# Kernel optimization log

Measured on AMD Instinct MI355X. Metric: run time of the kernel, lower is better.

The kernel has to match this reference:

```python
import jax, jax.numpy as jnp
import numpy as np

H = W = 32
C = 384
NH = 12
HEAD = C // NH
SCALE = HEAD ** -0.5
WS = 8            # window size
SS = 4            # shift size
N = WS * WS       # tokens per window (64)
NW = (H // WS) * (W // WS)  # windows per image (16)
HIDDEN = 4 * C
EPS = 1e-5
SQRT_2_OVER_PI = float(np.sqrt(2.0 / np.pi))


def _relative_position_index():
    ch = np.arange(WS)
    coords = np.stack(np.meshgrid(ch, ch, indexing='ij')).reshape(2, -1)  # [2, N]
    rel = (coords[:, :, None] - coords[:, None, :]).transpose(1, 2, 0)    # [N, N, 2]
    rel[:, :, 0] += WS - 1
    rel[:, :, 1] += WS - 1
    rel[:, :, 0] *= 2 * WS - 1
    return rel.sum(-1)  # [N, N] int


def _attn_mask():
    img = np.zeros((H, W), np.float32)
    sl = (slice(0, -WS), slice(-WS, -SS), slice(-SS, None))
    cnt = 0
    for hs in sl:
        for ws_ in sl:
            img[hs, ws_] = cnt
            cnt += 1
    m = img.reshape(H // WS, WS, W // WS, WS).transpose(0, 2, 1, 3).reshape(-1, N)  # [nW, N]
    am = m[:, None, :] - m[:, :, None]
    return np.where(am != 0, -100.0, 0.0).astype(np.float32)  # [nW, N, N]


REL_IDX = jnp.asarray(_relative_position_index())
ATTN_MASK = jnp.asarray(_attn_mask())


def _gelu(x):
    return x * 0.5 * (1.0 + jnp.tanh(SQRT_2_OVER_PI * (x + 0.044715 * x ** 3)))


def _layernorm(x, g, b):
    mu = jnp.mean(x, axis=-1, keepdims=True)
    var = jnp.mean(jnp.square(x - mu), axis=-1, keepdims=True)
    return (x - mu) * jax.lax.rsqrt(var + EPS) * g + b


def _window_partition(x):  # [B,H,W,C] -> [B*nW, N, C]
    B = x.shape[0]
    x = x.reshape(B, H // WS, WS, W // WS, WS, C).transpose(0, 1, 3, 2, 4, 5)
    return x.reshape(-1, N, C)


def _window_reverse(w, B):  # [B*nW, N, C] -> [B,H,W,C]
    x = w.reshape(B, H // WS, W // WS, WS, WS, C).transpose(0, 1, 3, 2, 4, 5)
    return x.reshape(B, H, W, C)


def setup_inputs() -> dict:
    key = jax.random.key(0)
    ks = jax.random.split(key, 16)
    s = 0.02
    return {
        'x': jax.random.normal(ks[0], (32, H * W, C), jnp.float32),
        'norm1_g': jnp.ones((C,), jnp.float32),
        'norm1_b': jnp.zeros((C,), jnp.float32),
        'qkv_w': jax.random.normal(ks[1], (C, 3 * C), jnp.float32) * s,
        'qkv_b': jnp.zeros((3 * C,), jnp.float32),
        'rel_bias_table': jax.random.normal(ks[2], ((2 * WS - 1) ** 2, NH), jnp.float32) * s,
        'proj_w': jax.random.normal(ks[3], (C, C), jnp.float32) * s,
        'proj_b': jnp.zeros((C,), jnp.float32),
        'norm2_g': jnp.ones((C,), jnp.float32),
        'norm2_b': jnp.zeros((C,), jnp.float32),
        'fc1_w': jax.random.normal(ks[4], (C, HIDDEN), jnp.float32) * s,
        'fc1_b': jnp.zeros((HIDDEN,), jnp.float32),
        'fc2_w': jax.random.normal(ks[5], (HIDDEN, C), jnp.float32) * s,
        'fc2_b': jnp.zeros((C,), jnp.float32),
    }


def reference(x, norm1_g, norm1_b, qkv_w, qkv_b, rel_bias_table, proj_w, proj_b,
              norm2_g, norm2_b, fc1_w, fc1_b, fc2_w, fc2_b):
    B = x.shape[0]
    shortcut = x
    y = _layernorm(x, norm1_g, norm1_b).reshape(B, H, W, C)
    y = jnp.roll(y, shift=(-SS, -SS), axis=(1, 2))          # cyclic shift
    win = _window_partition(y)                               # [B*nW, N, C]

    qkv = (win @ qkv_w + qkv_b).reshape(-1, N, 3, NH, HEAD).transpose(2, 0, 3, 1, 4)
    q, k, v = qkv[0], qkv[1], qkv[2]                         # [B*nW, NH, N, HEAD]
    attn = jnp.einsum('whnd,whmd->whnm', q * SCALE, k)       # [B*nW, NH, N, N]

    bias = rel_bias_table[REL_IDX.reshape(-1)].reshape(N, N, NH).transpose(2, 0, 1)
    attn = attn + bias[None]
    attn = attn.reshape(B, NW, NH, N, N) + ATTN_MASK[None, :, None]
    attn = jax.nn.softmax(attn.reshape(-1, NH, N, N), axis=-1)

    out = jnp.einsum('whnm,whmd->wnhd', attn, v).reshape(-1, N, C)
    out = out @ proj_w + proj_b                              # [B*nW, N, C]

    y = _window_reverse(out, B)
    y = jnp.roll(y, shift=(SS, SS), axis=(1, 2)).reshape(B, H * W, C)

    x = shortcut + y                                         # drop_path is identity (eval)
    h = _layernorm(x, norm2_g, norm2_b)
    h = _gelu(h @ fc1_w + fc1_b) @ fc2_w + fc2_b
    return x + h
```

## Files before the change

kernel.cpp:

```cpp
#include <hip/hip_runtime.h>
#include <hip/hip_bf16.h>
#include <math.h>

typedef __hip_bfloat16 bf16;
typedef __attribute__((ext_vector_type(8))) short short8;
typedef __attribute__((ext_vector_type(4))) float floatx4;

static constexpr int TOK = 32768;
static constexpr int CDIM = 384;
static constexpr int HID = 1536;

__device__ __forceinline__ bf16 f2bf(float v) { return __float2bfloat16(v); }

__device__ __forceinline__ unsigned short bf_bits(float a) {
  bf16 h = __float2bfloat16(a);
  unsigned short u;
  __builtin_memcpy(&u, &h, 2);
  return u;
}
__device__ __forceinline__ unsigned pack2(float a, float b) {
  return (unsigned)bf_bits(a) | ((unsigned)bf_bits(b) << 16);
}

typedef const __attribute__((address_space(1))) unsigned gas_t;
typedef __attribute__((address_space(3))) unsigned las_t;
__device__ __forceinline__ void gload16(const bf16* g, const bf16* l) {
  __builtin_amdgcn_global_load_lds((gas_t*)g, (las_t*)l, 16, 0, 0);
}

__global__ __launch_bounds__(256) void k_convt4(
    const float* __restrict__ s0, bf16* __restrict__ d0,
    const float* __restrict__ s1, bf16* __restrict__ d1,
    const float* __restrict__ s2, bf16* __restrict__ d2,
    const float* __restrict__ s3, bf16* __restrict__ d3) {
  int tid = blockIdx.x * 256 + threadIdx.x;
  const float* src; bf16* dst; int Kd, Nd, off;
  if (tid < 442368) { src = s0; dst = d0; Kd = 384; Nd = 1152; off = tid; }
  else if (tid < 589824) { src = s1; dst = d1; Kd = 384; Nd = 384; off = tid - 442368; }
  else if (tid < 1179648) { src = s2; dst = d2; Kd = 384; Nd = 1536; off = tid - 589824; }
  else { src = s3; dst = d3; Kd = 1536; Nd = 384; off = tid - 1179648; }
  int k = off / Nd, n = off - k * Nd;
  dst[(size_t)n * Kd + k] = f2bf(src[off]);
}

__global__ __launch_bounds__(256) void k_ln1(const float* __restrict__ x,
                                             const float* __restrict__ g,
                                             const float* __restrict__ b,
                                             bf16* __restrict__ out) {
  int wt = blockIdx.x * 4 + (threadIdx.x >> 6);
  int lane = threadIdx.x & 63;
  int win = wt >> 6, ntok = wt & 63;
  int bimg = win >> 4, wi = win & 15;
  int sh = (((wi >> 2) << 3) + (ntok >> 3) + 4) & 31;
  int sw = (((wi & 3) << 3) + (ntok & 7) + 4) & 31;
  const float* xr = x + ((size_t)bimg * 1024 + sh * 32 + sw) * CDIM;
  float v[6]; float s = 0.f, ss = 0.f;
#pragma unroll
  for (int j = 0; j < 6; ++j) {
    float t = xr[j * 64 + lane];
    v[j] = t; s += t; ss += t * t;
  }
#pragma unroll
  for (int off = 32; off > 0; off >>= 1) {
    s += __shfl_xor(s, off, 64);
    ss += __shfl_xor(ss, off, 64);
  }
  float mu = s * (1.f / 384.f);
  float var = ss * (1.f / 384.f) - mu * mu;
  float rs = rsqrtf(var + 1e-5f);
  bf16* orow = out + (size_t)wt * CDIM;
#pragma unroll
  for (int j = 0; j < 6; ++j) {
    int c = j * 64 + lane;
    orow[c] = f2bf((v[j] - mu) * rs * g[c] + b[c]);
  }
}

__global__ __launch_bounds__(256) void k_ln2(const float* __restrict__ x1,
                                             const float* __restrict__ g,
                                             const float* __restrict__ b,
                                             bf16* __restrict__ out) {
  int t = blockIdx.x * 4 + (threadIdx.x >> 6);
  int lane = threadIdx.x & 63;
  const float* xr = x1 + (size_t)t * CDIM;
  float v[6]; float s = 0.f, ss = 0.f;
#pragma unroll
  for (int j = 0; j < 6; ++j) {
    float q = xr[j * 64 + lane];
    v[j] = q; s += q; ss += q * q;
  }
#pragma unroll
  for (int off = 32; off > 0; off >>= 1) {
    s += __shfl_xor(s, off, 64);
    ss += __shfl_xor(ss, off, 64);
  }
  float mu = s * (1.f / 384.f);
  float var = ss * (1.f / 384.f) - mu * mu;
  float rs = rsqrtf(var + 1e-5f);
  bf16* orow = out + (size_t)t * CDIM;
#pragma unroll
  for (int j = 0; j < 6; ++j) {
    int c = j * 64 + lane;
    orow[c] = f2bf((v[j] - mu) * rs * g[c] + b[c]);
  }
}

template <int K, int EPI, int NT>
__global__ __launch_bounds__(256) void k_gemm(const bf16* __restrict__ A,
                                              const bf16* __restrict__ Bt,
                                              const float* __restrict__ bias,
                                              const float* __restrict__ extra,
                                              void* __restrict__ outp) {
  __shared__ __attribute__((aligned(16))) char pool[49152];
  bf16* A0 = (bf16*)pool;
  bf16* B0 = (bf16*)(pool + 8192);
  bf16* A1 = (bf16*)(pool + 16384);
  bf16* B1 = (bf16*)(pool + 24576);
  bf16* A2 = (bf16*)(pool + 32768);
  bf16* B2 = (bf16*)(pool + 40960);

  const int tid = threadIdx.x;
  const int wv = tid >> 6, lane = tid & 63;

  const int flat = blockIdx.x;
  const int xcd = flat & 7;
  const int idx = flat >> 3;
  const int rpx = (gridDim.x >> 3) / NT;
  const int cb = idx % NT;
  const int rb = idx / NT;
  const int mblk = (xcd * rpx + rb) * 128, nblk = cb * 128;

  const int srow = lane >> 3;
  const int sc = (lane & 7) ^ srow;
  const int srow2 = 2 * srow + (sc >> 2);
  const int gco = (sc & 3) * 8;
  const bf16* gaw = A + (size_t)(mblk + wv * 32 + srow2) * K + gco;
  const bf16* gbw = Bt + (size_t)(nblk + wv * 32 + srow2) * K + gco;
  bf16* lA0 = A0 + wv * 1024; bf16* lB0 = B0 + wv * 1024;
  bf16* lA1 = A1 + wv * 1024; bf16* lB1 = B1 + wv * 1024;
  bf16* lA2 = A2 + wv * 1024; bf16* lB2 = B2 + wv * 1024;

  const int wr = wv >> 1, wc = wv & 1;
  const int mr = lane & 15, q = lane >> 4;
  const int slot8 = ((((mr & 1) << 2) | q) ^ (mr >> 1)) * 8;
  const int faOff = (wr * 32 + (mr >> 1)) * 64 + slot8;
  const int fbOff = (wc * 32 + (mr >> 1)) * 64 + slot8;

  floatx4 acc[4][4];
#pragma unroll
  for (int i = 0; i < 4; ++i)
#pragma unroll
    for (int j = 0; j < 4; ++j) acc[i][j] = floatx4{0.f, 0.f, 0.f, 0.f};

#define VM4() asm volatile("s_waitcnt vmcnt(4)" ::: "memory")
#define VM0() asm volatile("s_waitcnt vmcnt(0)" ::: "memory")
#define BAR() __builtin_amdgcn_s_barrier()

#define STAGE(LA, LB, KOFF) do { \
    gload16(gaw + (KOFF), (LA)); \
    gload16(gaw + (KOFF) + 16 * K, (LA) + 512); \
    gload16(gbw + (KOFF), (LB)); \
    gload16(gbw + (KOFF) + 16 * K, (LB) + 512); \
  } while (0)

#define COMPUTE(ABASE, BBASE) do { \
    short8 a_[4], b_[4]; \
    _Pragma("unroll") \
    for (int mt = 0; mt < 4; ++mt) a_[mt] = *(const short8*)((ABASE) + faOff + mt * 512); \
    _Pragma("unroll") \
    for (int nt = 0; nt < 4; ++nt) b_[nt] = *(const short8*)((BBASE) + fbOff + nt * 512); \
    _Pragma("unroll") \
    for (int mt = 0; mt < 4; ++mt) \
      _Pragma("unroll") \
      for (int nt = 0; nt < 4; ++nt) \
        acc[mt][nt] = __builtin_amdgcn_mfma_f32_16x16x32_bf16(a_[mt], b_[nt], acc[mt][nt], 0, 0, 0); \
  } while (0)

  STAGE(lA0, lB0, 0);
  STAGE(lA1, lB1, 32);
  for (int k0 = 0; k0 < K - 96; k0 += 96) {
    VM4(); BAR(); STAGE(lA2, lB2, k0 + 64);  COMPUTE(A0, B0);
    VM4(); BAR(); STAGE(lA0, lB0, k0 + 96);  COMPUTE(A1, B1);
    VM4(); BAR(); STAGE(lA1, lB1, k0 + 128); COMPUTE(A2, B2);
  }
  VM4(); BAR(); STAGE(lA2, lB2, K - 32); COMPUTE(A0, B0);
  VM4(); BAR();                          COMPUTE(A1, B1);
  VM0(); BAR();                          COMPUTE(A2, B2);
#undef STAGE
#undef COMPUTE
#undef VM4
#undef VM0
#undef BAR

  __syncthreads();
  float* epsw = (float*)pool + wv * (16 * 68);
  const int rr = lane >> 2, c0 = (lane & 3) * 16;
#pragma unroll
  for (int mt = 0; mt < 4; ++mt) {
#pragma unroll
    for (int nt = 0; nt < 4; ++nt)
#pragma unroll
      for (int r = 0; r < 4; ++r)
        epsw[(q * 4 + r) * 68 + nt * 16 + mr] = acc[mt][nt][r];
    float v[16];
#pragma unroll
    for (int j = 0; j < 4; ++j) {
      float4 t = *(const float4*)&epsw[rr * 68 + c0 + j * 4];
      v[j * 4 + 0] = t.x; v[j * 4 + 1] = t.y; v[j * 4 + 2] = t.z; v[j * 4 + 3] = t.w;
    }
    const int grow = mblk + wr * 64 + mt * 16 + rr;
    const int gcol = nblk + wc * 64 + c0;

    if constexpr (EPI == 0) {
      int win = grow >> 6, ntok = grow & 63;
      int s = gcol / 384;
      int rem = gcol - s * 384;
      int h = rem >> 5, d0 = rem & 31;
      bf16* op = (bf16*)outp + (((size_t)s * 512 + win) * 12 + h) * 2048 + ntok * 32 + d0;
      uint4 pk;
      float bv[16];
#pragma unroll
      for (int j = 0; j < 16; ++j) bv[j] = v[j] + bias[gcol + j];
      pk.x = pack2(bv[0], bv[1]); pk.y = pack2(bv[2], bv[3]);
      pk.z = pack2(bv[4], bv[5]); pk.w = pack2(bv[6], bv[7]);
      *(uint4*)op = pk;
      pk.x = pack2(bv[8], bv[9]); pk.y = pack2(bv[10], bv[11]);
      pk.z = pack2(bv[12], bv[13]); pk.w = pack2(bv[14], bv[15]);
      *(uint4*)(op + 8) = pk;
    } else if constexpr (EPI == 1) {
      int win = grow >> 6, ntok = grow & 63;
      int bimg = win >> 4, wi = win & 15;
      int hh = (((wi >> 2) << 3) + (ntok >> 3) + 4) & 31;
      int ww = (((wi & 3) << 3) + (ntok & 7) + 4) & 31;
      size_t t = (size_t)bimg * 1024 + hh * 32 + ww;
      float* op = (float*)outp + t * CDIM + gcol;
      const float* xr = extra + t * CDIM + gcol;
#pragma unroll
      for (int j = 0; j < 4; ++j) {
        float4 xv = *(const float4*)(xr + j * 4);
        float4 ov;
        ov.x = xv.x + v[j * 4 + 0] + bias[gcol + j * 4 + 0];
        ov.y = xv.y + v[j * 4 + 1] + bias[gcol + j * 4 + 1];
        ov.z = xv.z + v[j * 4 + 2] + bias[gcol + j * 4 + 2];
        ov.w = xv.w + v[j * 4 + 3] + bias[gcol + j * 4 + 3];
        *(float4*)(op + j * 4) = ov;
      }
    }
  }
}

__global__ __launch_bounds__(512, 2) void k_mlp(const bf16* __restrict__ A,
                                                const bf16* __restrict__ W1t,
                                                const bf16* __restrict__ W2t,
                                                const float* __restrict__ b1,
                                                const float* __restrict__ b2,
                                                const float* __restrict__ x1,
                                                float* __restrict__ out) {
  __shared__ __attribute__((aligned(16))) char pool[131072];
  bf16* A0 = (bf16*)pool;
  bf16* A1 = (bf16*)(pool + 8192);
  bf16* A2 = (bf16*)(pool + 16384);
  bf16* W10 = (bf16*)(pool + 24576);
  bf16* W11 = (bf16*)(pool + 32768);
  bf16* W12 = (bf16*)(pool + 40960);
  bf16* hs = (bf16*)(pool + 49152);
  bf16* W2sA = (bf16*)(pool + 81920);
  bf16* W2sB = (bf16*)(pool + 106496);

  const int tid = threadIdx.x;
  const int wv = tid >> 6, lane = tid & 63;
  const int mblk = blockIdx.x * 128;

  const int srow = lane >> 3;
  const int sc = (lane & 7) ^ srow;
  const int srow2 = 2 * srow + (sc >> 2);
  const int gco = (sc & 3) * 8;

  const bf16* ga = A + (size_t)(mblk + wv * 16 + srow2) * 384 + gco;
  const bf16* g1 = W1t + (size_t)(wv * 16 + srow2) * 384 + gco;
  const bf16* g2 = W2t + (size_t)(wv * 48 + srow2) * 1536 + gco;

  const int wr1 = wv >> 2, wc1 = wv & 3;
  const int mr = lane & 15, q = lane >> 4;
  const int slot8 = ((((mr & 1) << 2) | q) ^ (mr >> 1)) * 8;
  const int faOff1 = (wr1 * 32 + (mr >> 1)) * 64 + slot8;
  const int fbOff1 = (wc1 * 16 + (mr >> 1)) * 64 + slot8;
  const int fbOff2 = (wc1 * 48 + (mr >> 1)) * 64 + slot8;
  const size_t hb = (size_t)(wr1 * 64 + mr) * 128;
  int px[4];
#pragma unroll
  for (int kk = 0; kk < 4; ++kk)
    px[kk] = (((kk & 2) << 2) | ((((kk & 1) << 2) | q) ^ (mr & 7))) * 8;

  floatx4 acc1[4][2];
  floatx4 acc2[4][6];
#pragma unroll
  for (int i = 0; i < 4; ++i) {
#pragma unroll
    for (int j = 0; j < 2; ++j) acc1[i][j] = floatx4{0.f, 0.f, 0.f, 0.f};
#pragma unroll
    for (int j = 0; j < 6; ++j) acc2[i][j] = floatx4{0.f, 0.f, 0.f, 0.f};
  }

#define VMW(N) asm volatile("s_waitcnt vmcnt(" #N ")" ::: "memory")
#define LGKM0() asm volatile("s_waitcnt lgkmcnt(0)" ::: "memory")
#define BARR() __builtin_amdgcn_s_barrier()
#define ST(ABUF, WBUF, G1P, KO) do { \
    gload16(ga + (KO), (ABUF) + wv * 512); \
    gload16((G1P) + (KO), (WBUF) + wv * 512); \
  } while (0)
#define STW2(BUF, KK) do { \
    _Pragma("unroll") \
    for (int g = 0; g < 3; ++g) \
      gload16(g2 + (KK) * 32 + (size_t)g * 16 * 1536, (BUF) + wv * 1536 + g * 512); \
  } while (0)
#define C1(AB, WB) do { \
    short8 a_[4], b_[2]; \
    _Pragma("unroll") \
    for (int mt = 0; mt < 4; ++mt) a_[mt] = *(const short8*)((AB) + faOff1 + mt * 512); \
    b_[0] = *(const short8*)((WB) + fbOff1); \
    b_[1] = *(const short8*)((WB) + fbOff1 + 512); \
    _Pragma("unroll") \
    for (int mt = 0; mt < 4; ++mt) \
      _Pragma("unroll") \
      for (int nt = 0; nt < 2; ++nt) \
        acc1[mt][nt] = __builtin_amdgcn_mfma_f32_16x16x32_bf16(a_[mt], b_[nt], acc1[mt][nt], 0, 0, 0); \
  } while (0)
#define C2(BUF, KK) do { \
    short8 ha[4], wb[6]; \
    _Pragma("unroll") \
    for (int mt = 0; mt < 4; ++mt) \
      ha[mt] = *(const short8*)(hs + hb + mt * 2048 + px[KK]); \
    _Pragma("unroll") \
    for (int nt = 0; nt < 6; ++nt) \
      wb[nt] = *(const short8*)((BUF) + fbOff2 + nt * 512); \
    _Pragma("unroll") \
    for (int mt = 0; mt < 4; ++mt) \
      _Pragma("unroll") \
      for (int nt = 0; nt < 6; ++nt) \
        acc2[mt][nt] = __builtin_amdgcn_mfma_f32_16x16x32_bf16(ha[mt], wb[nt], acc2[mt][nt], 0, 0, 0); \
  } while (0)
#define GELU_H(BB0, BB1) do { \
    _Pragma("unroll") \
    for (int mt = 0; mt < 4; ++mt) { \
      const int tokb = wr1 * 64 + mt * 16 + q * 4; \
      _Pragma("unroll") \
      for (int nt = 0; nt < 2; ++nt) { \
        const float bb = nt ? (BB1) : (BB0); \
        const int sw = wc1 * 4 + nt * 2 + (mr >> 3); \
        const int s8 = sw & 8, s7 = sw & 7; \
        _Pragma("unroll") \
        for (int r = 0; r < 4; ++r) { \
          float z = acc1[mt][nt][r] + bb; \
          float t2 = z * z; \
          float cp = __builtin_fmaf(t2, -0.0713548162f, -1.5957691216f); \
          float e = __expf(z * cp); \
          float gl = z * __builtin_amdgcn_rcpf(1.f + e); \
          const int t7 = ((q & 1) << 2) | r; \
          hs[(size_t)(tokb + r) * 128 + (s8 | (s7 ^ t7)) * 8 + (mr & 7)] = f2bf(gl); \
        } \
        acc1[mt][nt] = floatx4{0.f, 0.f, 0.f, 0.f}; \
      } \
    } \
    LGKM0(); \
  } while (0)

  ST(A0, W10, g1, 0);
  ST(A1, W11, g1, 32);

  for (int ci = 0; ci < 12; ++ci) {
    BARR();
    const int cb = ci * 128;
    float bb0 = b1[cb + wc1 * 32 + mr];
    float bb1 = b1[cb + wc1 * 32 + 16 + mr];
    STW2(W2sA, 0);

    const bf16* g1n = g1 + 49152;
    VMW(5); BARR(); ST(A2, W12, g1, 64);   C1(A0, W10);
    VMW(5); BARR(); ST(A0, W10, g1, 96);   C1(A1, W11);
    VMW(2); BARR(); ST(A1, W11, g1, 128);  C1(A2, W12);
    VMW(2); BARR(); ST(A2, W12, g1, 160);  C1(A0, W10);
    VMW(2); BARR(); ST(A0, W10, g1, 192);  C1(A1, W11);
    VMW(2); BARR(); ST(A1, W11, g1, 224);  C1(A2, W12);
    VMW(2); BARR(); ST(A2, W12, g1, 256);  C1(A0, W10);
    VMW(2); BARR(); ST(A0, W10, g1, 288);  C1(A1, W11);
    VMW(2); BARR(); ST(A1, W11, g1, 320);  C1(A2, W12);
    VMW(2); BARR(); ST(A2, W12, g1, 352);  C1(A0, W10);
    VMW(2); BARR(); ST(A0, W10, g1n, 0);   C1(A1, W11);
    VMW(2); BARR(); ST(A1, W11, g1n, 32);  C1(A2, W12);

    GELU_H(bb0, bb1);
    __syncthreads();

    STW2(W2sB, 1);
    C2(W2sA, 0);
    BARR();
    STW2(W2sA, 2);
    VMW(3); BARR();
    C2(W2sB, 1);
    BARR();
    STW2(W2sB, 3);
    VMW(3); BARR();
    C2(W2sA, 2);
    VMW(0); BARR();
    C2(W2sB, 3);

    g1 += 49152;
    g2 += 128;
  }
#undef ST
#undef STW2
#undef C1
#undef C2
#undef GELU_H

  VMW(0);
  __syncthreads();

  float* epsw = (float*)(pool + wv * 6400);
  const int rr = lane >> 2, c4 = (lane & 3) * 24;
#pragma unroll
  for (int mt = 0; mt < 4; ++mt) {
#pragma unroll
    for (int nt = 0; nt < 6; ++nt)
#pragma unroll
      for (int r = 0; r < 4; ++r)
        epsw[(q * 4 + r) * 100 + nt * 16 + mr] = acc2[mt][nt][r];
    const int grow = mblk + wr1 * 64 + mt * 16 + rr;
    const int gcol = wc1 * 96 + c4;
    const float* xr = x1 + (size_t)grow * 384 + gcol;
    float* op = out + (size_t)grow * 384 + gcol;
#pragma unroll
    for (int j = 0; j < 6; ++j) {
      float4 t = *(const float4*)&epsw[rr * 100 + c4 + j * 4];
      float4 xv = *(const float4*)(xr + j * 4);
      float4 bv = *(const float4*)&b2[gcol + j * 4];
      float4 ov;
      ov.x = xv.x + t.x + bv.x;
      ov.y = xv.y + t.y + bv.y;
      ov.z = xv.z + t.z + bv.z;
      ov.w = xv.w + t.w + bv.w;
      *(float4*)(op + j * 4) = ov;
    }
  }
#undef VMW
#undef LGKM0
#undef BARR
}

__global__ __launch_bounds__(64) void k_attn(const bf16* __restrict__ qkv,
                                             const float* __restrict__ tblg,
                                             bf16* __restrict__ out) {
  __shared__ __attribute__((aligned(16))) char pool[16384];
  bf16* Qs = (bf16*)pool;
  bf16* Ks = (bf16*)(pool + 5120);
  bf16* Ps = (bf16*)pool;
  float* Os = (float*)pool;
  bf16* Vt = (bf16*)(pool + 10240);
  unsigned long long* msk = (unsigned long long*)(pool + 14848);
  float* tbl = (float*)(pool + 15360);

  const int bid = blockIdx.x;
  const int win = bid / 12, head = bid - win * 12;
  const int lane = threadIdx.x;
  const int q = lane >> 4, mr = lane & 15;

  for (int i = lane; i < 225; i += 64) tbl[i] = tblg[i * 12 + head];

  size_t base = ((size_t)win * 12 + head) * 2048 + lane * 32;
  const uint4* qp = (const uint4*)(qkv + base);
  const uint4* kp = (const uint4*)(qkv + (size_t)12582912 + base);
  const uint4* vp = (const uint4*)(qkv + (size_t)25165824 + base);
#pragma unroll
  for (int i = 0; i < 4; ++i) *(uint4*)(Qs + lane * 40 + i * 8) = qp[i];
#pragma unroll
  for (int i = 0; i < 4; ++i) *(uint4*)(Ks + lane * 40 + i * 8) = kp[i];
  {
    union { uint4 u[4]; unsigned short h[32]; } vv;
#pragma unroll
    for (int i = 0; i < 4; ++i) vv.u[i] = vp[i];
    unsigned short* VtU = (unsigned short*)Vt;
#pragma unroll
    for (int d = 0; d < 32; ++d) VtU[d * 72 + lane] = vv.h[d];
  }
  {
    int wi = win & 15;
    int ri = lane >> 3, ci = lane & 7;
    int rh = ((wi >> 2) << 3) + ri, rw = ((wi & 3) << 3) + ci;
    int rid = (rh < 24 ? 0 : (rh < 28 ? 1 : 2)) * 3 + (rw < 24 ? 0 : (rw < 28 ? 1 : 2));
    unsigned long long m = 0;
#pragma unroll
    for (int v = 0; v < 9; ++v) {
      unsigned long long bb = __ballot(rid == v);
      if (rid == v) m = bb;
    }
    msk[lane] = m;
  }

  floatx4 sac[4][4];
#pragma unroll
  for (int i = 0; i < 4; ++i)
#pragma unroll
    for (int j = 0; j < 4; ++j) sac[i][j] = floatx4{0.f, 0.f, 0.f, 0.f};
  {
    short8 af[4], bf[4];
#pragma unroll
    for (int t = 0; t < 4; ++t) af[t] = *(const short8*)(Qs + (t * 16 + mr) * 40 + q * 8);
#pragma unroll
    for (int t = 0; t < 4; ++t) bf[t] = *(const short8*)(Ks + (t * 16 + mr) * 40 + q * 8);
#pragma unroll
    for (int mt = 0; mt < 4; ++mt)
#pragma unroll
      for (int nt = 0; nt < 4; ++nt)
        sac[mt][nt] = __builtin_amdgcn_mfma_f32_16x16x32_bf16(af[mt], bf[nt], sac[mt][nt], 0, 0, 0);
  }

  float psum[4][4];
#pragma unroll
  for (int mt = 0; mt < 4; ++mt)
#pragma unroll
    for (int r = 0; r < 4; ++r) psum[mt][r] = 0.f;
#pragma unroll
  for (int mt = 0; mt < 4; ++mt) {
#pragma unroll
    for (int r = 0; r < 4; ++r) {
      const int i = mt * 16 + q * 4 + r;
      const unsigned long long mrow = msk[i];
      const int bi = (i >> 3) * 15 + (i & 7);
#pragma unroll
      for (int nt = 0; nt < 4; ++nt) {
        const int j = nt * 16 + mr;
        const int idx = bi + 112 - (j >> 3) * 15 - (j & 7);
        float val = sac[mt][nt][r] * 0.17677669529663687f + tbl[idx];
        float p = __expf(val);
        p = ((mrow >> j) & 1ull) ? p : 0.f;
        psum[mt][r] += p;
        Ps[i * 72 + j] = f2bf(p);
      }
    }
  }
  float inv[4][4];
#pragma unroll
  for (int mt = 0; mt < 4; ++mt)
#pragma unroll
    for (int r = 0; r < 4; ++r) {
      float s = psum[mt][r];
      s += __shfl_xor(s, 1, 64);
      s += __shfl_xor(s, 2, 64);
      s += __shfl_xor(s, 4, 64);
      s += __shfl_xor(s, 8, 64);
      inv[mt][r] = 1.f / s;
    }

  floatx4 oac[4][2];
#pragma unroll
  for (int i = 0; i < 4; ++i)
#pragma unroll
    for (int j = 0; j < 2; ++j) oac[i][j] = floatx4{0.f, 0.f, 0.f, 0.f};
#pragma unroll
  for (int kk = 0; kk < 2; ++kk) {
    short8 ap[4], bv[2];
#pragma unroll
    for (int mt = 0; mt < 4; ++mt)
      ap[mt] = *(const short8*)(Ps + (mt * 16 + mr) * 72 + kk * 32 + q * 8);
#pragma unroll
    for (int nt = 0; nt < 2; ++nt)
      bv[nt] = *(const short8*)(Vt + (nt * 16 + mr) * 72 + kk * 32 + q * 8);
#pragma unroll
    for (int mt = 0; mt < 4; ++mt)
#pragma unroll
      for (int nt = 0; nt < 2; ++nt)
        oac[mt][nt] = __builtin_amdgcn_mfma_f32_16x16x32_bf16(ap[mt], bv[nt], oac[mt][nt], 0, 0, 0);
  }

#pragma unroll
  for (int mt = 0; mt < 4; ++mt)
#pragma unroll
    for (int nt = 0; nt < 2; ++nt)
#pragma unroll
      for (int r = 0; r < 4; ++r)
        Os[(mt * 16 + q * 4 + r) * 40 + nt * 16 + mr] = oac[mt][nt][r] * inv[mt][r];
  float ov[32];
#pragma unroll
  for (int c = 0; c < 8; ++c) {
    const int cc = c ^ (lane & 7);
    float4 t = *(const float4*)(Os + lane * 40 + cc * 4);
    ov[cc * 4 + 0] = t.x; ov[cc * 4 + 1] = t.y;
    ov[cc * 4 + 2] = t.z; ov[cc * 4 + 3] = t.w;
  }
  uint4* o4 = (uint4*)(out + ((size_t)win * 64 + lane) * CDIM + head * 32);
#pragma unroll
  for (int i = 0; i < 4; ++i) {
    uint4 pk;
    pk.x = pack2(ov[i * 8 + 0], ov[i * 8 + 1]);
    pk.y = pack2(ov[i * 8 + 2], ov[i * 8 + 3]);
    pk.z = pack2(ov[i * 8 + 4], ov[i * 8 + 5]);
    pk.w = pack2(ov[i * 8 + 6], ov[i * 8 + 7]);
    o4[i] = pk;
  }
}

extern "C" void kernel_launch(void* const* d_in, const int* in_sizes, int n_in,
                              void* d_out, int out_size, void* d_ws, size_t ws_size,
                              hipStream_t stream) {
  const float* x = (const float*)d_in[0];
  const float* n1g = (const float*)d_in[1];
  const float* n1b = (const float*)d_in[2];
  const float* qkv_w = (const float*)d_in[3];
  const float* qkv_b = (const float*)d_in[4];
  const float* reltbl = (const float*)d_in[5];
  const float* proj_w = (const float*)d_in[6];
  const float* proj_b = (const float*)d_in[7];
  const float* n2g = (const float*)d_in[8];
  const float* n2b = (const float*)d_in[9];
  const float* fc1_w = (const float*)d_in[10];
  const float* fc1_b = (const float*)d_in[11];
  const float* fc2_w = (const float*)d_in[12];
  const float* fc2_b = (const float*)d_in[13];
  float* out = (float*)d_out;

  char* p = (char*)d_ws;
  bf16* w_qkv_t = (bf16*)p;  p += (size_t)442368 * 2;
  bf16* w_proj_t = (bf16*)p; p += (size_t)147456 * 2;
  bf16* w_fc1_t = (bf16*)p;  p += (size_t)589824 * 2;
  bf16* w_fc2_t = (bf16*)p;  p += (size_t)589824 * 2;
  bf16* bufA = (bf16*)p;     p += (size_t)12582912 * 2;
  bf16* qkvb = (bf16*)p;     p += (size_t)37748736 * 2;
  bf16* attno = (bf16*)p;    p += (size_t)12582912 * 2;
  float* x1 = (float*)p;     p += (size_t)12582912 * 4;

  k_convt4<<<dim3(6912), dim3(256), 0, stream>>>(qkv_w, w_qkv_t, proj_w, w_proj_t,
                                                 fc1_w, w_fc1_t, fc2_w, w_fc2_t);

  k_ln1<<<dim3(8192), dim3(256), 0, stream>>>(x, n1g, n1b, bufA);
  k_gemm<384, 0, 9><<<dim3(9 * 256), dim3(256), 0, stream>>>(bufA, w_qkv_t, qkv_b, nullptr, qkvb);
  k_attn<<<dim3(6144), dim3(64), 0, stream>>>(qkvb, reltbl, attno);
  k_gemm<384, 1, 3><<<dim3(3 * 256), dim3(256), 0, stream>>>(attno, w_proj_t, proj_b, x, x1);
  k_ln2<<<dim3(8192), dim3(256), 0, stream>>>(x1, n2g, n2b, bufA);
  k_mlp<<<dim3(256), dim3(512), 0, stream>>>(bufA, w_fc1_t, w_fc2_t, fc1_b, fc2_b, x1, out);
}
```

Measured before the change: 388.4 us.

## Store residual x1 in bf16 and merge weight conversion with LN1 launch

The intermediate residual x1 produced by the projection GEMM is now stored as bf16 instead of fp32, and LN2 and the MLP epilogue read it back as bf16. This halves the bytes written and read for that tensor, at the cost of extra rounding on the residual stream that the final output depends on. The weight transpose/convert kernel and the LN1 kernel are also merged into one launch to remove a kernel boundary.

```diff
diff --git a/kernel.cpp b/kernel.cpp
--- a/kernel.cpp
+++ b/kernel.cpp
@@ -21,6 +21,12 @@
 __device__ __forceinline__ unsigned pack2(float a, float b) {
   return (unsigned)bf_bits(a) | ((unsigned)bf_bits(b) << 16);
 }
+__device__ __forceinline__ float bfl(unsigned u) {
+  unsigned w = u << 16; float f; __builtin_memcpy(&f, &w, 4); return f;
+}
+__device__ __forceinline__ float bfh(unsigned u) {
+  unsigned w = u & 0xffff0000u; float f; __builtin_memcpy(&f, &w, 4); return f;
+}
 
 typedef const __attribute__((address_space(1))) unsigned gas_t;
 typedef __attribute__((address_space(3))) unsigned las_t;
@@ -28,26 +34,25 @@
   __builtin_amdgcn_global_load_lds((gas_t*)g, (las_t*)l, 16, 0, 0);
 }
 
-__global__ __launch_bounds__(256) void k_convt4(
+__global__ __launch_bounds__(256) void k_pre(
     const float* __restrict__ s0, bf16* __restrict__ d0,
     const float* __restrict__ s1, bf16* __restrict__ d1,
     const float* __restrict__ s2, bf16* __restrict__ d2,
-    const float* __restrict__ s3, bf16* __restrict__ d3) {
-  int tid = blockIdx.x * 256 + threadIdx.x;
-  const float* src; bf16* dst; int Kd, Nd, off;
-  if (tid < 442368) { src = s0; dst = d0; Kd = 384; Nd = 1152; off = tid; }
-  else if (tid < 589824) { src = s1; dst = d1; Kd = 384; Nd = 384; off = tid - 442368; }
-  else if (tid < 1179648) { src = s2; dst = d2; Kd = 384; Nd = 1536; off = tid - 589824; }
-  else { src = s3; dst = d3; Kd = 1536; Nd = 384; off = tid - 1179648; }
-  int k = off / Nd, n = off - k * Nd;
-  dst[(size_t)n * Kd + k] = f2bf(src[off]);
-}
-
-__global__ __launch_bounds__(256) void k_ln1(const float* __restrict__ x,
-                                             const float* __restrict__ g,
-                                             const float* __restrict__ b,
-                                             bf16* __restrict__ out) {
-  int wt = blockIdx.x * 4 + (threadIdx.x >> 6);
+    const float* __restrict__ s3, bf16* __restrict__ d3,
+    const float* __restrict__ x, const float* __restrict__ g,
+    const float* __restrict__ b, bf16* __restrict__ out) {
+  if (blockIdx.x < 6912) {
+    int tid = blockIdx.x * 256 + threadIdx.x;
+    const float* src; bf16* dst; int Kd, Nd, off;
+    if (tid < 442368) { src = s0; dst = d0; Kd = 384; Nd = 1152; off = tid; }
+    else if (tid < 589824) { src = s1; dst = d1; Kd = 384; Nd = 384; off = tid - 442368; }
+    else if (tid < 1179648) { src = s2; dst = d2; Kd = 384; Nd = 1536; off = tid - 589824; }
+    else { src = s3; dst = d3; Kd = 1536; Nd = 384; off = tid - 1179648; }
+    int k = off / Nd, n = off - k * Nd;
+    dst[(size_t)n * Kd + k] = f2bf(src[off]);
+    return;
+  }
+  int wt = (blockIdx.x - 6912) * 4 + (threadIdx.x >> 6);
   int lane = threadIdx.x & 63;
   int win = wt >> 6, ntok = wt & 63;
   int bimg = win >> 4, wi = win & 15;
@@ -76,17 +81,17 @@
   }
 }
 
-__global__ __launch_bounds__(256) void k_ln2(const float* __restrict__ x1,
+__global__ __launch_bounds__(256) void k_ln2(const bf16* __restrict__ x1,
                                              const float* __restrict__ g,
                                              const float* __restrict__ b,
                                              bf16* __restrict__ out) {
   int t = blockIdx.x * 4 + (threadIdx.x >> 6);
   int lane = threadIdx.x & 63;
-  const float* xr = x1 + (size_t)t * CDIM;
+  const bf16* xr = x1 + (size_t)t * CDIM;
   float v[6]; float s = 0.f, ss = 0.f;
 #pragma unroll
   for (int j = 0; j < 6; ++j) {
-    float q = xr[j * 64 + lane];
+    float q = __bfloat162float(xr[j * 64 + lane]);
     v[j] = q; s += q; ss += q * q;
   }
 #pragma unroll
@@ -233,18 +238,24 @@
       int hh = (((wi >> 2) << 3) + (ntok >> 3) + 4) & 31;
       int ww = (((wi & 3) << 3) + (ntok & 7) + 4) & 31;
       size_t t = (size_t)bimg * 1024 + hh * 32 + ww;
-      float* op = (float*)outp + t * CDIM + gcol;
+      bf16* op = (bf16*)outp + t * CDIM + gcol;
       const float* xr = extra + t * CDIM + gcol;
+      float ov[16];
 #pragma unroll
       for (int j = 0; j < 4; ++j) {
         float4 xv = *(const float4*)(xr + j * 4);
-        float4 ov;
-        ov.x = xv.x + v[j * 4 + 0] + bias[gcol + j * 4 + 0];
-        ov.y = xv.y + v[j * 4 + 1] + bias[gcol + j * 4 + 1];
-        ov.z = xv.z + v[j * 4 + 2] + bias[gcol + j * 4 + 2];
-        ov.w = xv.w + v[j * 4 + 3] + bias[gcol + j * 4 + 3];
-        *(float4*)(op + j * 4) = ov;
+        ov[j * 4 + 0] = xv.x + v[j * 4 + 0] + bias[gcol + j * 4 + 0];
+        ov[j * 4 + 1] = xv.y + v[j * 4 + 1] + bias[gcol + j * 4 + 1];
+        ov[j * 4 + 2] = xv.z + v[j * 4 + 2] + bias[gcol + j * 4 + 2];
+        ov[j * 4 + 3] = xv.w + v[j * 4 + 3] + bias[gcol + j * 4 + 3];
       }
+      uint4 pk;
+      pk.x = pack2(ov[0], ov[1]); pk.y = pack2(ov[2], ov[3]);
+      pk.z = pack2(ov[4], ov[5]); pk.w = pack2(ov[6], ov[7]);
+      *(uint4*)op = pk;
+      pk.x = pack2(ov[8], ov[9]); pk.y = pack2(ov[10], ov[11]);
+      pk.z = pack2(ov[12], ov[13]); pk.w = pack2(ov[14], ov[15]);
+      *(uint4*)(op + 8) = pk;
     }
   }
 }
@@ -254,7 +265,7 @@
                                                 const bf16* __restrict__ W2t,
                                                 const float* __restrict__ b1,
                                                 const float* __restrict__ b2,
-                                                const float* __restrict__ x1,
+                                                const bf16* __restrict__ x1,
                                                 float* __restrict__ out) {
   __shared__ __attribute__((aligned(16))) char pool[131072];
   bf16* A0 = (bf16*)pool;
@@ -428,18 +439,26 @@
         epsw[(q * 4 + r) * 100 + nt * 16 + mr] = acc2[mt][nt][r];
     const int grow = mblk + wr1 * 64 + mt * 16 + rr;
     const int gcol = wc1 * 96 + c4;
-    const float* xr = x1 + (size_t)grow * 384 + gcol;
+    const bf16* xr = x1 + (size_t)grow * 384 + gcol;
     float* op = out + (size_t)grow * 384 + gcol;
+    float xv[24];
+#pragma unroll
+    for (int j3 = 0; j3 < 3; ++j3) {
+      uint4 xp = *(const uint4*)(xr + j3 * 8);
+      xv[j3 * 8 + 0] = bfl(xp.x); xv[j3 * 8 + 1] = bfh(xp.x);
+      xv[j3 * 8 + 2] = bfl(xp.y); xv[j3 * 8 + 3] = bfh(xp.y);
+      xv[j3 * 8 + 4] = bfl(xp.z); xv[j3 * 8 + 5] = bfh(xp.z);
+      xv[j3 * 8 + 6] = bfl(xp.w); xv[j3 * 8 + 7] = bfh(xp.w);
+    }
 #pragma unroll
     for (int j = 0; j < 6; ++j) {
       float4 t = *(const float4*)&epsw[rr * 100 + c4 + j * 4];
-      float4 xv = *(const float4*)(xr + j * 4);
       float4 bv = *(const float4*)&b2[gcol + j * 4];
       float4 ov;
-      ov.x = xv.x + t.x + bv.x;
-      ov.y = xv.y + t.y + bv.y;
-      ov.z = xv.z + t.z + bv.z;
-      ov.w = xv.w + t.w + bv.w;
+      ov.x = xv[j * 4 + 0] + t.x + bv.x;
+      ov.y = xv[j * 4 + 1] + t.y + bv.y;
+      ov.z = xv[j * 4 + 2] + t.z + bv.z;
+      ov.w = xv[j * 4 + 3] + t.w + bv.w;
       *(float4*)(op + j * 4) = ov;
     }
   }
@@ -627,12 +646,12 @@
   bf16* bufA = (bf16*)p;     p += (size_t)12582912 * 2;
   bf16* qkvb = (bf16*)p;     p += (size_t)37748736 * 2;
   bf16* attno = (bf16*)p;    p += (size_t)12582912 * 2;
-  float* x1 = (float*)p;     p += (size_t)12582912 * 4;
-
-  k_convt4<<<dim3(6912), dim3(256), 0, stream>>>(qkv_w, w_qkv_t, proj_w, w_proj_t,
-                                                 fc1_w, w_fc1_t, fc2_w, w_fc2_t);
-
-  k_ln1<<<dim3(8192), dim3(256), 0, stream>>>(x, n1g, n1b, bufA);
+  bf16* x1 = (bf16*)p;       p += (size_t)12582912 * 2;
+
+  k_pre<<<dim3(15104), dim3(256), 0, stream>>>(qkv_w, w_qkv_t, proj_w, w_proj_t,
+                                               fc1_w, w_fc1_t, fc2_w, w_fc2_t,
+                                               x, n1g, n1b, bufA);
+
   k_gemm<384, 0, 9><<<dim3(9 * 256), dim3(256), 0, stream>>>(bufA, w_qkv_t, qkv_b, nullptr, qkvb);
   k_attn<<<dim3(6144), dim3(64), 0, stream>>>(qkvb, reltbl, attno);
   k_gemm<384, 1, 3><<<dim3(3 * 256), dim3(256), 0, stream>>>(attno, w_proj_t, proj_b, x, x1);
```

Result: faster. 372.4 us (-4.1%).
